# Kernel optimization log

Hardware: AMD Instinct MI355X
Metric: run time of the kernel (lower is better)

The kernel has to match this reference:

```python
import jax, jax.numpy as jnp
import numpy as np

FIVE = 6            # top-k features kept per output unit
OUT, IN, HID, B = 512, 1024, 32, 256


def setup_inputs() -> dict:
    key = jax.random.key(0)
    ks = jax.random.split(key, 6)
    return {
        "inputs": jax.random.normal(ks[0], (B, IN), jnp.float32),
        "mask": jax.random.normal(ks[1], (OUT, IN), jnp.float32),
        "W1": jax.random.normal(ks[2], (OUT, IN, HID), jnp.float32) / 2.236,
        "W2": jax.random.normal(ks[3], (OUT, HID, HID), jnp.float32) / HID ** 0.5,
        "W3": jax.random.normal(ks[4], (OUT, HID, HID), jnp.float32) / HID ** 0.5,
        "W4": jax.random.normal(ks[5], (OUT, HID, 1), jnp.float32) / HID ** 0.5,
    }


def reference(inputs, mask, W1, W2, W3, W4):
    # top-k binary mask: 1 at the FIVE largest entries of each row of mask
    _, idx = jax.lax.top_k(mask, FIVE)                       # (out, FIVE)
    rows = jnp.arange(mask.shape[0])[:, None]
    m = jnp.zeros_like(mask).at[rows, idx].set(1.0)          # (out, in)

    # gated inputs, broadcast of torch's bmm outer-product trick:
    # x[o,b,i] = inputs[b,i] * m[o,i]
    x = inputs[None, :, :] * m[:, None, :]                   # (out, batch, in)

    # per-output-unit 4-layer MLP (batched over 'o')
    h = jax.nn.relu(jnp.einsum('obi,oih->obh', x, W1))       # (out, batch, hid)
    h = jax.nn.relu(jnp.einsum('obh,ohk->obk', h, W2))
    h = jax.nn.relu(jnp.einsum('obh,ohk->obk', h, W3))
    y = jnp.einsum('obh,oh->ob', h, W4[:, :, 0])             # (out, batch)
    y = jax.nn.sigmoid(y).T                                  # (batch, out)

    # STE binarize (forward value)
    q = (y >= 0.5).astype(y.dtype) * 2.0 - 1.0
    return q
```

## Files before the change

kernel.cpp:

```cpp
#include <hip/hip_runtime.h>
#include <math.h>

#define NOUT 512
#define NIN  1024
#define HID  32
#define NB   256
#define TOPK 6
#define HSTR 40

typedef _Float16 f16x8 __attribute__((ext_vector_type(8)));
typedef float    f32x4 __attribute__((ext_vector_type(4)));

union HU  { _Float16 h; unsigned short u; };
union H4U { _Float16 h[4]; unsigned long long u; };
union H8U { _Float16 h[8]; uint4 u; };

__device__ __forceinline__ unsigned short f16bits(float v) {
    HU c; c.h = (_Float16)v; return c.u;
}

template<int NMT>
__device__ __forceinline__ void mfma_layer(
    const unsigned short* WtHi, const unsigned short* WtLo,
    const unsigned short* HHi,  const unsigned short* HLo,
    int lane15, int quad, int wb, f32x4 acc[NMT][4])
{
    f16x8 aH[NMT], aL[NMT], bH[4], bL[4];
#pragma unroll
    for (int mt = 0; mt < NMT; ++mt) {
        int off = (mt * 16 + lane15) * HSTR + quad * 8;
        aH[mt] = *(const f16x8*)&WtHi[off];
        aL[mt] = *(const f16x8*)&WtLo[off];
    }
#pragma unroll
    for (int nt = 0; nt < 4; ++nt) {
        int off = (wb + nt * 16 + lane15) * HSTR + quad * 8;
        bH[nt] = *(const f16x8*)&HHi[off];
        bL[nt] = *(const f16x8*)&HLo[off];
    }
#pragma unroll
    for (int mt = 0; mt < NMT; ++mt)
#pragma unroll
        for (int nt = 0; nt < 4; ++nt) {
            acc[mt][nt] = __builtin_amdgcn_mfma_f32_16x16x32_f16(aH[mt], bH[nt], acc[mt][nt], 0, 0, 0);
            acc[mt][nt] = __builtin_amdgcn_mfma_f32_16x16x32_f16(aH[mt], bL[nt], acc[mt][nt], 0, 0, 0);
            acc[mt][nt] = __builtin_amdgcn_mfma_f32_16x16x32_f16(aL[mt], bH[nt], acc[mt][nt], 0, 0, 0);
            acc[mt][nt] = __builtin_amdgcn_mfma_f32_16x16x32_f16(aL[mt], bL[nt], acc[mt][nt], 0, 0, 0);
        }
}

__device__ __forceinline__ void store_h(
    unsigned short* HHi, unsigned short* HLo,
    int lane15, int quad, int wb, f32x4 acc[2][4])
{
#pragma unroll
    for (int mt = 0; mt < 2; ++mt)
#pragma unroll
        for (int nt = 0; nt < 4; ++nt) {
            H4U hi, lo;
#pragma unroll
            for (int r = 0; r < 4; ++r) {
                float v = acc[mt][nt][r];
                v = v > 0.0f ? v : 0.0f;
                _Float16 h = (_Float16)v;
                hi.h[r] = h;
                lo.h[r] = (_Float16)(v - (float)h);
            }
            int off = (wb + nt * 16 + lane15) * HSTR + mt * 16 + quad * 4;
            *(unsigned long long*)&HHi[off] = hi.u;
            *(unsigned long long*)&HLo[off] = lo.u;
        }
}

__global__ __launch_bounds__(256, 2) void blayer_kernel(
    const float* __restrict__ inputs,
    const float* __restrict__ mask,
    const float* __restrict__ W1,
    const float* __restrict__ W2,
    const float* __restrict__ W3,
    const float* __restrict__ W4,
    float* __restrict__ out)
{
    const int o = blockIdx.x;
    const int t = threadIdx.x;
    const int l = t & 63, lane15 = l & 15, quad = l >> 4;
    const int wb = (t >> 6) * 64;

    __shared__ __align__(16) unsigned short HtHi[NB * HSTR];
    __shared__ __align__(16) unsigned short HtLo[NB * HSTR];
    __shared__ __align__(16) unsigned short WHi[3][HID * HSTR];
    __shared__ __align__(16) unsigned short WLo[3][HID * HSTR];
    __shared__ __align__(16) unsigned short W4Hi[16 * HSTR];
    __shared__ __align__(16) unsigned short W4Lo[16 * HSTR];
    __shared__ float vals[NIN];
    __shared__ int   sidx[TOPK];
    __shared__ float red_v[4];
    __shared__ int   red_i[4];

    const float* W2g = W2 + (size_t)o * HID * HID;
    const float* W3g = W3 + (size_t)o * HID * HID;
    const float* W4g = W4 + (size_t)o * HID;
    const float* W1g = W1 + (size_t)o * NIN * HID;

#pragma unroll
    for (int i = 0; i < 4; ++i) {
        int e = t + i * 256, m = e & 31, k = e >> 5;
        float v2 = W2g[e], v3 = W3g[e];
        _Float16 h2 = (_Float16)v2, h3 = (_Float16)v3;
        WHi[1][m * HSTR + k] = f16bits(v2);
        WLo[1][m * HSTR + k] = f16bits(v2 - (float)h2);
        WHi[2][m * HSTR + k] = f16bits(v3);
        WLo[2][m * HSTR + k] = f16bits(v3 - (float)h3);
    }
#pragma unroll
    for (int i = 0; i < 2; ++i) {
        int e = t + i * 256, m = e >> 5, k = e & 31;
        float v = (m == 0) ? W4g[k] : 0.0f;
        _Float16 h = (_Float16)v;
        W4Hi[m * HSTR + k] = f16bits(v);
        W4Lo[m * HSTR + k] = f16bits(v - (float)h);
    }

    const float* mrow = mask + (size_t)o * NIN;
#pragma unroll
    for (int k = 0; k < NIN / NB; ++k) vals[t + NB * k] = mrow[t + NB * k];
    __syncthreads();

    for (int it = 0; it < TOPK; ++it) {
        float bv = -INFINITY;
        int   bi = 0;
#pragma unroll
        for (int k = 0; k < NIN / NB; ++k) {
            float v = vals[t + NB * k];
            if (v > bv) { bv = v; bi = t + NB * k; }
        }
#pragma unroll
        for (int off = 32; off > 0; off >>= 1) {
            float ov = __shfl_down(bv, off);
            int   oi = __shfl_down(bi, off);
            if (ov > bv) { bv = ov; bi = oi; }
        }
        if ((t & 63) == 0) { red_v[t >> 6] = bv; red_i[t >> 6] = bi; }
        __syncthreads();
        if (t == 0) {
            float fv = red_v[0]; int fi = red_i[0];
            for (int w = 1; w < 4; ++w)
                if (red_v[w] > fv) { fv = red_v[w]; fi = red_i[w]; }
            sidx[it] = fi;
            vals[fi] = -INFINITY;
        }
        __syncthreads();
    }

#pragma unroll
    for (int i = 0; i < 4; ++i) {
        int e = t + i * 256, m = e & 31, k = e >> 5;
        float v = (k < TOPK) ? W1g[(size_t)sidx[k] * HID + m] : 0.0f;
        _Float16 h = (_Float16)v;
        WHi[0][m * HSTR + k] = f16bits(v);
        WLo[0][m * HSTR + k] = f16bits(v - (float)h);
    }

    {
        int sj[TOPK];
#pragma unroll
        for (int j = 0; j < TOPK; ++j)
            sj[j] = __builtin_amdgcn_readfirstlane(sidx[j]);
        H8U xh, xl;
#pragma unroll
        for (int j = 0; j < 8; ++j) { xh.h[j] = (_Float16)0.0f; xl.h[j] = (_Float16)0.0f; }
#pragma unroll
        for (int j = 0; j < TOPK; ++j) {
            float v = inputs[(size_t)t * NIN + sj[j]];
            _Float16 h = (_Float16)v;
            xh.h[j] = h;
            xl.h[j] = (_Float16)(v - (float)h);
        }
        *(uint4*)&HtHi[t * HSTR]      = xh.u;
        *(uint4*)&HtLo[t * HSTR]      = xl.u;
        uint4 z = make_uint4(0, 0, 0, 0);
        *(uint4*)&HtHi[t * HSTR + 8]  = z;
        *(uint4*)&HtHi[t * HSTR + 16] = z;
        *(uint4*)&HtHi[t * HSTR + 24] = z;
        *(uint4*)&HtLo[t * HSTR + 8]  = z;
        *(uint4*)&HtLo[t * HSTR + 16] = z;
        *(uint4*)&HtLo[t * HSTR + 24] = z;
    }
    __syncthreads();

    f32x4 acc[2][4];
#pragma unroll
    for (int L = 0; L < 3; ++L) {
#pragma unroll
        for (int mt = 0; mt < 2; ++mt)
#pragma unroll
            for (int nt = 0; nt < 4; ++nt) acc[mt][nt] = (f32x4){0.f, 0.f, 0.f, 0.f};
        mfma_layer<2>(&WHi[L][0], &WLo[L][0], HtHi, HtLo, lane15, quad, wb, acc);
        store_h(HtHi, HtLo, lane15, quad, wb, acc);
    }

    f32x4 acc4[1][4];
#pragma unroll
    for (int nt = 0; nt < 4; ++nt) acc4[0][nt] = (f32x4){0.f, 0.f, 0.f, 0.f};
    mfma_layer<1>(W4Hi, W4Lo, HtHi, HtLo, lane15, quad, wb, acc4);

    if (quad == 0) {
#pragma unroll
        for (int nt = 0; nt < 4; ++nt) {
            int b = wb + nt * 16 + lane15;
            out[(size_t)b * NOUT + o] = (acc4[0][nt][0] >= 0.0f) ? 1.0f : -1.0f;
        }
    }
}

extern "C" void kernel_launch(void* const* d_in, const int* in_sizes, int n_in,
                              void* d_out, int out_size, void* d_ws, size_t ws_size,
                              hipStream_t stream) {
    const float* inputs = (const float*)d_in[0];
    const float* mask   = (const float*)d_in[1];
    const float* W1     = (const float*)d_in[2];
    const float* W2     = (const float*)d_in[3];
    const float* W3     = (const float*)d_in[4];
    const float* W4     = (const float*)d_in[5];
    float* out = (float*)d_out;

    blayer_kernel<<<dim3(NOUT), dim3(NB), 0, stream>>>(
        inputs, mask, W1, W2, W3, W4, out);
}
```

Before: 112.3 us.

## Split top-k into separate kernel and halve batch per MLP block

Top-k selection moves into its own kernel, where one wavefront per output row keeps the row in registers and reduces with shuffles, so the block-wide barriers and shared-memory reductions are gone. The MLP kernel then reads the indices from workspace and runs two 128-thread blocks per output unit, each handling half the batch, which doubles the grid and raises occupancy. Input gathers are issued early, before the weight staging. The cost is an extra kernel launch, a workspace round-trip, and W1/W2/W3 staging repeated in each half-block.

Result: slower. 115.4 us (+2.8%).

```diff
diff --git a/kernel.cpp b/kernel.cpp
--- a/kernel.cpp
+++ b/kernel.cpp
@@ -17,6 +17,37 @@
 
 __device__ __forceinline__ unsigned short f16bits(float v) {
     HU c; c.h = (_Float16)v; return c.u;
+}
+
+__global__ __launch_bounds__(256) void topk_kernel(
+    const float* __restrict__ mask, int* __restrict__ sidx_out)
+{
+    const int o = (blockIdx.x << 2) | (threadIdx.x >> 6);
+    const int l = threadIdx.x & 63;
+    const float* mrow = mask + (size_t)o * NIN;
+
+    float v[16];
+#pragma unroll
+    for (int j = 0; j < 16; ++j) v[j] = mrow[j * 64 + l];
+
+#pragma unroll
+    for (int it = 0; it < TOPK; ++it) {
+        float bv = v[0]; int bi = l;
+#pragma unroll
+        for (int j = 1; j < 16; ++j)
+            if (v[j] > bv) { bv = v[j]; bi = j * 64 + l; }
+#pragma unroll
+        for (int off = 32; off; off >>= 1) {
+            float ov = __shfl_down(bv, off);
+            int   oi = __shfl_down(bi, off);
+            if (ov > bv) { bv = ov; bi = oi; }
+        }
+        bi = __shfl(bi, 0);
+#pragma unroll
+        for (int j = 0; j < 16; ++j)
+            if (bi == j * 64 + l) v[j] = -INFINITY;
+        if (l == 0) sidx_out[o * 8 + it] = bi;
+    }
 }
 
 template<int NMT>
@@ -72,39 +103,55 @@
         }
 }
 
-__global__ __launch_bounds__(256, 2) void blayer_kernel(
+__global__ __launch_bounds__(128, 4) void mlp_kernel(
     const float* __restrict__ inputs,
-    const float* __restrict__ mask,
     const float* __restrict__ W1,
     const float* __restrict__ W2,
     const float* __restrict__ W3,
     const float* __restrict__ W4,
+    const int*   __restrict__ sidxg,
     float* __restrict__ out)
 {
-    const int o = blockIdx.x;
-    const int t = threadIdx.x;
+    const int o    = blockIdx.x >> 1;
+    const int half = (blockIdx.x & 1) << 7;
+    const int t    = threadIdx.x;
     const int l = t & 63, lane15 = l & 15, quad = l >> 4;
-    const int wb = (t >> 6) * 64;
-
-    __shared__ __align__(16) unsigned short HtHi[NB * HSTR];
-    __shared__ __align__(16) unsigned short HtLo[NB * HSTR];
+    const int wb = (t >> 6) << 6;
+
+    __shared__ __align__(16) unsigned short HtHi[128 * HSTR];
+    __shared__ __align__(16) unsigned short HtLo[128 * HSTR];
     __shared__ __align__(16) unsigned short WHi[3][HID * HSTR];
     __shared__ __align__(16) unsigned short WLo[3][HID * HSTR];
     __shared__ __align__(16) unsigned short W4Hi[16 * HSTR];
     __shared__ __align__(16) unsigned short W4Lo[16 * HSTR];
-    __shared__ float vals[NIN];
-    __shared__ int   sidx[TOPK];
-    __shared__ float red_v[4];
-    __shared__ int   red_i[4];
-
+
+    int sj[TOPK];
+#pragma unroll
+    for (int j = 0; j < TOPK; ++j)
+        sj[j] = __builtin_amdgcn_readfirstlane(sidxg[o * 8 + j]);
+
+    const int bglob = half + t;
+    float xg[TOPK];
+#pragma unroll
+    for (int j = 0; j < TOPK; ++j)
+        xg[j] = inputs[(size_t)bglob * NIN + sj[j]];
+
+    const float* W1g = W1 + (size_t)o * NIN * HID;
     const float* W2g = W2 + (size_t)o * HID * HID;
     const float* W3g = W3 + (size_t)o * HID * HID;
     const float* W4g = W4 + (size_t)o * HID;
-    const float* W1g = W1 + (size_t)o * NIN * HID;
-
-#pragma unroll
-    for (int i = 0; i < 4; ++i) {
-        int e = t + i * 256, m = e & 31, k = e >> 5;
+
+#pragma unroll
+    for (int i = 0; i < 8; ++i) {
+        int e = t + i * 128, m = e & 31, k = e >> 5;
+        float v = (k < TOPK) ? W1g[(size_t)sj[k] * HID + m] : 0.0f;
+        _Float16 h = (_Float16)v;
+        WHi[0][m * HSTR + k] = f16bits(v);
+        WLo[0][m * HSTR + k] = f16bits(v - (float)h);
+    }
+#pragma unroll
+    for (int i = 0; i < 8; ++i) {
+        int e = t + i * 128, m = e & 31, k = e >> 5;
         float v2 = W2g[e], v3 = W3g[e];
         _Float16 h2 = (_Float16)v2, h3 = (_Float16)v3;
         WHi[1][m * HSTR + k] = f16bits(v2);
@@ -113,65 +160,21 @@
         WLo[2][m * HSTR + k] = f16bits(v3 - (float)h3);
     }
 #pragma unroll
-    for (int i = 0; i < 2; ++i) {
-        int e = t + i * 256, m = e >> 5, k = e & 31;
+    for (int i = 0; i < 4; ++i) {
+        int e = t + i * 128, m = e >> 5, k = e & 31;
         float v = (m == 0) ? W4g[k] : 0.0f;
         _Float16 h = (_Float16)v;
         W4Hi[m * HSTR + k] = f16bits(v);
         W4Lo[m * HSTR + k] = f16bits(v - (float)h);
     }
 
-    const float* mrow = mask + (size_t)o * NIN;
-#pragma unroll
-    for (int k = 0; k < NIN / NB; ++k) vals[t + NB * k] = mrow[t + NB * k];
-    __syncthreads();
-
-    for (int it = 0; it < TOPK; ++it) {
-        float bv = -INFINITY;
-        int   bi = 0;
-#pragma unroll
-        for (int k = 0; k < NIN / NB; ++k) {
-            float v = vals[t + NB * k];
-            if (v > bv) { bv = v; bi = t + NB * k; }
-        }
-#pragma unroll
-        for (int off = 32; off > 0; off >>= 1) {
-            float ov = __shfl_down(bv, off);
-            int   oi = __shfl_down(bi, off);
-            if (ov > bv) { bv = ov; bi = oi; }
-        }
-        if ((t & 63) == 0) { red_v[t >> 6] = bv; red_i[t >> 6] = bi; }
-        __syncthreads();
-        if (t == 0) {
-            float fv = red_v[0]; int fi = red_i[0];
-            for (int w = 1; w < 4; ++w)
-                if (red_v[w] > fv) { fv = red_v[w]; fi = red_i[w]; }
-            sidx[it] = fi;
-            vals[fi] = -INFINITY;
-        }
-        __syncthreads();
-    }
-
-#pragma unroll
-    for (int i = 0; i < 4; ++i) {
-        int e = t + i * 256, m = e & 31, k = e >> 5;
-        float v = (k < TOPK) ? W1g[(size_t)sidx[k] * HID + m] : 0.0f;
-        _Float16 h = (_Float16)v;
-        WHi[0][m * HSTR + k] = f16bits(v);
-        WLo[0][m * HSTR + k] = f16bits(v - (float)h);
-    }
-
     {
-        int sj[TOPK];
-#pragma unroll
-        for (int j = 0; j < TOPK; ++j)
-            sj[j] = __builtin_amdgcn_readfirstlane(sidx[j]);
         H8U xh, xl;
 #pragma unroll
         for (int j = 0; j < 8; ++j) { xh.h[j] = (_Float16)0.0f; xl.h[j] = (_Float16)0.0f; }
 #pragma unroll
         for (int j = 0; j < TOPK; ++j) {
-            float v = inputs[(size_t)t * NIN + sj[j]];
+            float v = xg[j];
             _Float16 h = (_Float16)v;
             xh.h[j] = h;
             xl.h[j] = (_Float16)(v - (float)h);
@@ -207,7 +210,7 @@
     if (quad == 0) {
 #pragma unroll
         for (int nt = 0; nt < 4; ++nt) {
-            int b = wb + nt * 16 + lane15;
+            int b = half + wb + nt * 16 + lane15;
             out[(size_t)b * NOUT + o] = (acc4[0][nt][0] >= 0.0f) ? 1.0f : -1.0f;
         }
     }
@@ -222,8 +225,10 @@
     const float* W2     = (const float*)d_in[3];
     const float* W3     = (const float*)d_in[4];
     const float* W4     = (const float*)d_in[5];
-    float* out = (float*)d_out;
-
-    blayer_kernel<<<dim3(NOUT), dim3(NB), 0, stream>>>(
-        inputs, mask, W1, W2, W3, W4, out);
-}
+    float* out  = (float*)d_out;
+    int*   sidx = (int*)d_ws;
+
+    topk_kernel<<<dim3(NOUT / 4), dim3(256), 0, stream>>>(mask, sidx);
+    mlp_kernel<<<dim3(NOUT * 2), dim3(128), 0, stream>>>(
+        inputs, W1, W2, W3, W4, sidx, out);
+}
```
